# Kernel optimization log

Measured on AMD Instinct MI355X. Metric: run time of the kernel, lower is better.

## Reference

```python
import jax, jax.numpy as jnp
import numpy as np

B, T, C = 8, 2048, 512
H = 8
DH = C // H
MLP = 4 * C
EPS = 1e-5


def _ln(x, w, b):
    m = jnp.mean(x, axis=-1, keepdims=True)
    v = jnp.mean(jnp.square(x - m), axis=-1, keepdims=True)
    return (x - m) * jax.lax.rsqrt(v + EPS) * w + b


def setup_inputs() -> dict:
    key = jax.random.key(0)
    ks = jax.random.split(key, 12)
    s = 0.02
    return {
        "x": jax.random.normal(ks[0], (B, T, C), jnp.float32),
        "c": jax.random.normal(ks[1], (B, C), jnp.float32),
        "qkv_w": jax.random.normal(ks[2], (3 * C, C), jnp.float32) * s,
        "qkv_b": jnp.zeros((3 * C,), jnp.float32),
        "proj_w": jax.random.normal(ks[3], (C, C), jnp.float32) * s,
        "proj_b": jnp.zeros((C,), jnp.float32),
        "ada_w": jax.random.normal(ks[4], (6 * C, C), jnp.float32) * s,
        "ada_b": jnp.zeros((6 * C,), jnp.float32),
        "fc1_w": jax.random.normal(ks[5], (MLP, C), jnp.float32) * s,
        "fc1_b": jnp.zeros((MLP,), jnp.float32),
        "fc2_w": jax.random.normal(ks[6], (C, MLP), jnp.float32) * s,
        "fc2_b": jnp.zeros((C,), jnp.float32),
        "ln1_w": jnp.ones((C,), jnp.float32),
        "ln1_b": jnp.zeros((C,), jnp.float32),
        "ln2_w": jnp.ones((C,), jnp.float32),
        "ln2_b": jnp.zeros((C,), jnp.float32),
    }


def reference(x, c, qkv_w, qkv_b, proj_w, proj_b, ada_w, ada_b,
              fc1_w, fc1_b, fc2_w, fc2_b, ln1_w, ln1_b, ln2_w, ln2_b):
    # AdaLN modulation: SiLU -> Linear -> chunk into 6 [B,C] pieces
    mod = jax.nn.silu(c) @ ada_w.T + ada_b  # [B, 6C]
    sh_msa, sc_msa, g_msa, sh_mlp, sc_mlp, g_mlp = jnp.split(mod, 6, axis=1)

    # --- attention branch ---
    h = _ln(x, ln1_w, ln1_b) * (1.0 + sc_msa[:, None, :]) + sh_msa[:, None, :]
    qkv = h @ qkv_w.T + qkv_b  # [B, T, 3C]
    q, k, v = jnp.split(qkv, 3, axis=-1)
    q = q.reshape(B, T, H, DH).transpose(0, 2, 1, 3)  # [B,H,T,Dh]
    k = k.reshape(B, T, H, DH).transpose(0, 2, 1, 3)
    v = v.reshape(B, T, H, DH).transpose(0, 2, 1, 3)
    scores = jnp.einsum('bhqd,bhkd->bhqk', q, k) * (1.0 / np.sqrt(DH))
    w = jax.nn.softmax(scores, axis=-1)
    o = jnp.einsum('bhqk,bhkd->bhqd', w, v)  # [B,H,T,Dh]
    o = o.transpose(0, 2, 1, 3).reshape(B, T, C)
    attn = o @ proj_w.T + proj_b
    x = x + g_msa[:, None, :] * attn

    # --- MLP branch ---
    h2 = _ln(x, ln2_w, ln2_b) * (1.0 + sc_mlp[:, None, :]) + sh_mlp[:, None, :]
    m = jax.nn.gelu(h2 @ fc1_w.T + fc1_b, approximate=True) @ fc2_w.T + fc2_b
    return x + g_mlp[:, None, :] * m
```

## Files before the change

### kernel.cpp

```cpp
#include <hip/hip_runtime.h>
#include <cstdint>
#include <cstddef>

typedef unsigned short u16;
typedef short v8s __attribute__((ext_vector_type(8)));
typedef float v4f __attribute__((ext_vector_type(4)));
typedef float f32x16 __attribute__((ext_vector_type(16)));
typedef unsigned int v4u __attribute__((ext_vector_type(4)));
typedef unsigned short v4u16 __attribute__((ext_vector_type(4)));

#define TT 2048
#define CC 512

#define QSCALE 0.18033688011112042f

__device__ __forceinline__ u16 f2bf(float f) {
    unsigned u = __float_as_uint(f);
    u += 0x7fffu + ((u >> 16) & 1u);
    return (u16)(u >> 16);
}

__device__ __forceinline__ unsigned cvt_pk_bf16(float lo, float hi) {
    unsigned r;
    asm("v_cvt_pk_bf16_f32 %0, %1, %2" : "=v"(r) : "v"(lo), "v"(hi));
    return r;
}

__device__ __forceinline__ float fexp2(float x) {
    float xf = __builtin_floorf(x);
    float f = x - xf;
    float p = __builtin_fmaf(f, __builtin_fmaf(f, 0.343779f, 0.656213f), 1.0f);
    int e = (int)xf;
    return __uint_as_float(__float_as_uint(p) + ((unsigned)(e << 23)));
}

__device__ __forceinline__ void swap32(unsigned a, unsigned b, unsigned& x, unsigned& y) {
#if __has_builtin(__builtin_amdgcn_permlane32_swap)
    auto r = __builtin_amdgcn_permlane32_swap(a, b, false, false);
    x = r[0]; y = r[1];
#else
    unsigned bx = (unsigned)__shfl_xor((int)b, 32, 64);
    unsigned ax = (unsigned)__shfl_xor((int)a, 32, 64);
    bool hi5 = (threadIdx.x & 32) != 0;
    x = hi5 ? bx : a;
    y = hi5 ? b : ax;
#endif
}

__device__ __forceinline__ void gl2lds16(const void* g, void* l) {
    __builtin_amdgcn_global_load_lds(
        (const __attribute__((address_space(1))) unsigned int*)g,
        (__attribute__((address_space(3))) unsigned int*)l,
        16, 0, 0);
}

__global__ __launch_bounds__(256) void f2bf_all(const float* __restrict__ s0,
                                                const float* __restrict__ s1,
                                                const float* __restrict__ s2,
                                                const float* __restrict__ s3,
                                                u16* __restrict__ d) {
    int i = (blockIdx.x * 256 + threadIdx.x) * 4;
    const float* s; int off;
    if (i < 786432)       { s = s0; off = 0; }
    else if (i < 1048576) { s = s1; off = 786432; }
    else if (i < 2097152) { s = s2; off = 1048576; }
    else                  { s = s3; off = 2097152; }
    float4 v = *(const float4*)(s + (i - off));
    v4u16 r;
    r[0] = f2bf(v.x); r[1] = f2bf(v.y); r[2] = f2bf(v.z); r[3] = f2bf(v.w);
    *(v4u16*)(d + i) = r;
}

__global__ __launch_bounds__(256) void ada_kernel(const float* __restrict__ c,
                                                  const float* __restrict__ W,
                                                  const float* __restrict__ bias,
                                                  float* __restrict__ mod) {
    int idx = blockIdx.x * 4 + (threadIdx.x >> 6);
    int l = threadIdx.x & 63;
    int bb = idx / 3072;
    int n = idx - bb * 3072;
    const float* cp = c + bb * CC;
    const float* wp = W + (size_t)n * CC;
    float s = 0.f;
    #pragma unroll
    for (int i = 0; i < 8; ++i) {
        int k = l * 8 + i;
        float cv = cp[k];
        float sil = cv / (1.f + __expf(-cv));
        s += sil * wp[k];
    }
    #pragma unroll
    for (int off = 32; off; off >>= 1) s += __shfl_xor(s, off, 64);
    if (l == 0) mod[idx] = s + bias[n];
}

__global__ __launch_bounds__(256) void ln_mod_kernel(const float* __restrict__ X,
                                                     const float* __restrict__ lnw,
                                                     const float* __restrict__ lnb,
                                                     const float* __restrict__ mod,
                                                     int sh_off, int sc_off,
                                                     u16* __restrict__ out) {
    int row = blockIdx.x * 4 + (threadIdx.x >> 6);
    int l = threadIdx.x & 63;
    int b = row >> 11;
    const float* xr = X + (size_t)row * CC + l * 8;
    float4 va = *(const float4*)(xr);
    float4 vb = *(const float4*)(xr + 4);
    float v[8] = {va.x, va.y, va.z, va.w, vb.x, vb.y, vb.z, vb.w};
    float s = 0.f;
    #pragma unroll
    for (int i = 0; i < 8; ++i) s += v[i];
    #pragma unroll
    for (int off = 32; off; off >>= 1) s += __shfl_xor(s, off, 64);
    float mean = s * (1.f / CC);
    float q = 0.f;
    #pragma unroll
    for (int i = 0; i < 8; ++i) { float d = v[i] - mean; q += d * d; }
    #pragma unroll
    for (int off = 32; off; off >>= 1) q += __shfl_xor(q, off, 64);
    float rstd = rsqrtf(q * (1.f / CC) + 1e-5f);
    int col = l * 8;
    const float* shp = mod + b * 3072 + sh_off + col;
    const float* scp = mod + b * 3072 + sc_off + col;
    v8s st;
    #pragma unroll
    for (int i = 0; i < 8; ++i) {
        float hv = (v[i] - mean) * rstd * lnw[col + i] + lnb[col + i];
        float r = hv * (1.f + scp[i]) + shp[i];
        st[i] = (short)f2bf(r);
    }
    *(v8s*)(out + (size_t)row * CC + col) = st;
}

__global__ __launch_bounds__(512) void vt_kernel(const u16* __restrict__ qkv,
                                                 u16* __restrict__ vT) {
    __shared__ u16 tile[64 * 72];
    const int id = blockIdx.x;
    const int bh = id >> 5, tt = id & 31;
    const int b = bh >> 3, h = bh & 7;
    const int tid = threadIdx.x;
    const int tr = tid >> 3, d0 = (tid & 7) * 8;
    v8s v = *(const v8s*)(qkv + (size_t)(b * TT + tt * 64 + tr) * 1536 + 1024 + h * 64 + d0);
    *(v8s*)(&tile[tr * 72 + d0]) = v;
    __syncthreads();
    const int dr = tid >> 3, t0 = (tid & 7) * 8;
    v8s ov;
    #pragma unroll
    for (int e = 0; e < 8; ++e) ov[e] = (short)tile[(t0 + e) * 72 + dr];
    *(v8s*)(vT + (size_t)(bh * 64 + dr) * TT + tt * 64 + t0) = ov;
}

template <int MODE>
__global__ __launch_bounds__(512, 4)
void gemm_bt(const u16* __restrict__ A, const u16* __restrict__ W,
             const float* __restrict__ bias, void* __restrict__ outp,
             const float* __restrict__ resid, const float* __restrict__ gate,
             int NX, int N, int K) {
    __shared__ alignas(16) u16 Al[2][8192];
    __shared__ alignas(16) u16 Bl[2][4096];
    const int id = blockIdx.x;
    const int wg = (id & 7) * (gridDim.x >> 3) + (id >> 3);
    const int by = wg / NX, bx = wg - by * NX;
    const int bn = bx << 7, bm = by << 8;
    const int tid = threadIdx.x;
    const int w = tid >> 6, l = tid & 63;
    const int hi = l >> 4, lo = l & 15;
    const int wr = (w >> 1) << 6, wc = (w & 1) << 6;

    v4f acc[4][4] = {};

    const int srow = l >> 2;
    const int sp = l & 3;
    const int NT = K >> 5;

    auto stage = [&](int buf, int kt) {
        const int k0 = kt << 5;
        #pragma unroll
        for (int i = 0; i < 2; ++i) {
            const int c = w + (i << 3);
            const int row = (c << 4) + srow;
            const int lg = sp ^ ((row >> 1) & 3);
            gl2lds16(A + (size_t)(bm + row) * K + k0 + (lg << 3), &Al[buf][c << 9]);
        }
        {
            const int row = (w << 4) + srow;
            const int lg = sp ^ ((row >> 1) & 3);
            gl2lds16(W + (size_t)(bn + row) * K + k0 + (lg << 3), &Bl[buf][w << 9]);
        }
    };

    stage(0, 0);
    __syncthreads();
    int cur = 0;
    for (int t = 0; t < NT; ++t) {
        if (t + 1 < NT) stage(cur ^ 1, t + 1);
        const u16* Ab = Al[cur];
        const u16* Bb = Bl[cur];
        v8s aF[4], bF[4];
        #pragma unroll
        for (int mi = 0; mi < 4; ++mi) {
            int r = wr + (mi << 4) + lo;
            aF[mi] = *(const v8s*)(Ab + (r << 5) + ((hi ^ ((r >> 1) & 3)) << 3));
        }
        #pragma unroll
        for (int ni = 0; ni < 4; ++ni) {
            int r = wc + (ni << 4) + lo;
            bF[ni] = *(const v8s*)(Bb + (r << 5) + ((hi ^ ((r >> 1) & 3)) << 3));
        }
        #pragma unroll
        for (int mi = 0; mi < 4; ++mi)
            #pragma unroll
            for (int ni = 0; ni < 4; ++ni)
                acc[mi][ni] = __builtin_amdgcn_mfma_f32_16x16x32_bf16(
                    aF[mi], bF[ni], acc[mi][ni], 0, 0, 0);
        __syncthreads();
        cur ^= 1;
    }

    #pragma unroll
    for (int mi = 0; mi < 4; ++mi) {
        #pragma unroll
        for (int ni = 0; ni < 4; ++ni) {
            int col = bn + wc + (ni << 4) + lo;
            float bv = bias[col];
            #pragma unroll
            for (int j = 0; j < 4; ++j) {
                int row = bm + wr + (mi << 4) + hi * 4 + j;
                float v = acc[mi][ni][j] + bv;
                if constexpr (MODE == 0) {
                    float sc2 = (col < 512) ? QSCALE : 1.0f;
                    ((u16*)outp)[(size_t)row * N + col] = f2bf(v * sc2);
                } else if constexpr (MODE == 1) {
                    float u2 = 1.5957691216057308f * (v + 0.044715f * v * v * v);
                    float g = v / (1.f + __expf(-u2));
                    ((u16*)outp)[(size_t)row * N + col] = f2bf(g);
                } else {
                    float r = resid[(size_t)row * N + col];
                    float gt = gate[(row >> 11) * 3072 + col];
                    ((float*)outp)[(size_t)row * N + col] = r + gt * v;
                }
            }
        }
    }
}

__global__ __launch_bounds__(512, 4)
void attn_kernel(const u16* __restrict__ qkv, const u16* __restrict__ vT,
                 u16* __restrict__ O) {
    __shared__ alignas(16) u16 smem[18432];
    const int tid = threadIdx.x;
    const int w = tid >> 6, l = tid & 63;
    const int l31 = l & 31, l5 = l >> 5;
    const int id = blockIdx.x;
    const int bh = id & 63, b = bh >> 3, h = bh & 7;
    const int qt = id >> 6;

    const int qrow = qt * 256 + w * 32 + l31;
    const u16* qp = qkv + (size_t)(b * TT + qrow) * 1536 + h * 64;
    v8s qf[4];
    #pragma unroll
    for (int ks = 0; ks < 4; ++ks) qf[ks] = *(const v8s*)(qp + ks * 16 + l5 * 8);

    const int r8 = l >> 3;
    const int kc = (l & 7) ^ r8 ^ w;
    const u16* kptr = qkv + (size_t)(b * TT + 8 * w + r8) * 1536 + 512 + h * 64 + kc * 8;
    const u16* vptr = vT + (size_t)(bh * 64 + 8 * w + r8) * TT + kc * 8;

    auto stageKV = [&](int it, int buf) {
        gl2lds16(kptr + (size_t)it * 64 * 1536, smem + buf * 4096 + w * 512);
        gl2lds16(vptr + it * 64, smem + 8192 + buf * 4096 + w * 512);
    };

    const char* sbase = (const char*)smem;
    int offs[8];
    #pragma unroll
    for (int t = 0; t < 2; ++t)
        #pragma unroll
        for (int ks = 0; ks < 4; ++ks) {
            int row = t * 32 + l31;
            int phys = ((ks << 1) + l5) ^ (row & 7) ^ ((row >> 3) & 7);
            offs[t * 4 + ks] = row * 128 + phys * 16;
        }

    v8s onesf;
    #pragma unroll
    for (int i = 0; i < 8; ++i) onesf[i] = (short)0x3F80;

    stageKV(0, 0);
    __syncthreads();

    f32x16 o[2] = {};
    f32x16 lacc = {};

    #pragma unroll 2
    for (int it = 0; it < 32; ++it) {
        const int cur = it & 1;
        if (it + 1 < 32) stageKV(it + 1, cur ^ 1);
        const int koff = cur * 8192;

        f32x16 st[2];
        st[0] = (f32x16)0.f; st[1] = (f32x16)0.f;
        __builtin_amdgcn_s_setprio(1);
        #pragma unroll
        for (int ks = 0; ks < 4; ++ks) {
            v8s k0 = *(const v8s*)(sbase + offs[ks] + koff);
            v8s k1 = *(const v8s*)(sbase + offs[4 + ks] + koff);
            st[0] = __builtin_amdgcn_mfma_f32_32x32x16_bf16(k0, qf[ks], st[0], 0, 0, 0);
            st[1] = __builtin_amdgcn_mfma_f32_32x32x16_bf16(k1, qf[ks], st[1], 0, 0, 0);
        }
        __builtin_amdgcn_s_setprio(0);

        #pragma unroll
        for (int t2 = 0; t2 < 2; ++t2)
            #pragma unroll
            for (int r = 0; r < 16; ++r)
                st[t2][r] = fexp2(st[t2][r]);

        __builtin_amdgcn_s_setprio(1);
        #pragma unroll
        for (int ks = 0; ks < 4; ++ks) {
            const int tt = ks >> 1, rb = (ks & 1) * 8;
            unsigned pkA = cvt_pk_bf16(st[tt][rb + 0], st[tt][rb + 1]);
            unsigned pkB = cvt_pk_bf16(st[tt][rb + 4], st[tt][rb + 5]);
            unsigned pkC = cvt_pk_bf16(st[tt][rb + 2], st[tt][rb + 3]);
            unsigned pkD = cvt_pk_bf16(st[tt][rb + 6], st[tt][rb + 7]);
            unsigned w0, w1, w2, w3;
            swap32(pkA, pkB, w0, w2);
            swap32(pkC, pkD, w1, w3);
            v4u pw; pw[0] = w0; pw[1] = w1; pw[2] = w2; pw[3] = w3;
            v8s pa = __builtin_bit_cast(v8s, pw);
            v8s vf0 = *(const v8s*)(sbase + offs[ks] + koff + 16384);
            v8s vf1 = *(const v8s*)(sbase + offs[4 + ks] + koff + 16384);
            o[0] = __builtin_amdgcn_mfma_f32_32x32x16_bf16(vf0, pa, o[0], 0, 0, 0);
            o[1] = __builtin_amdgcn_mfma_f32_32x32x16_bf16(vf1, pa, o[1], 0, 0, 0);
            lacc = __builtin_amdgcn_mfma_f32_32x32x16_bf16(onesf, pa, lacc, 0, 0, 0);
        }
        __builtin_amdgcn_s_setprio(0);
        __syncthreads();
    }

    float inv = 1.f / lacc[0];
    char* outw = (char*)smem + w * 4608;
    #pragma unroll
    for (int t2 = 0; t2 < 2; ++t2)
        #pragma unroll
        for (int r = 0; r < 16; r += 2) {
            int dh = t2 * 32 + (r & 3) + ((r >> 2) << 3) + (l5 << 2);
            unsigned pk = cvt_pk_bf16(o[t2][r] * inv, o[t2][r + 1] * inv);
            *(unsigned*)(outw + l31 * 144 + dh * 2) = pk;
        }
    __syncthreads();
    #pragma unroll
    for (int i = 0; i < 4; ++i) {
        int idx = (i << 9) + tid;
        int qq = idx >> 3, cch = idx & 7;
        v8s vd = *(const v8s*)((char*)smem + (qq >> 5) * 4608 + (qq & 31) * 144 + cch * 16);
        *(v8s*)(O + (size_t)(b * TT + qt * 256 + qq) * 512 + h * 64 + cch * 8) = vd;
    }
}

extern "C" void kernel_launch(void* const* d_in, const int* in_sizes, int n_in,
                              void* d_out, int out_size, void* d_ws, size_t ws_size,
                              hipStream_t stream) {
    const float* x = (const float*)d_in[0];
    const float* c = (const float*)d_in[1];
    const float* qkv_w = (const float*)d_in[2];
    const float* qkv_b = (const float*)d_in[3];
    const float* proj_w = (const float*)d_in[4];
    const float* proj_b = (const float*)d_in[5];
    const float* ada_w = (const float*)d_in[6];
    const float* ada_b = (const float*)d_in[7];
    const float* fc1_w = (const float*)d_in[8];
    const float* fc1_b = (const float*)d_in[9];
    const float* fc2_w = (const float*)d_in[10];
    const float* fc2_b = (const float*)d_in[11];
    const float* ln1_w = (const float*)d_in[12];
    const float* ln1_b = (const float*)d_in[13];
    const float* ln2_w = (const float*)d_in[14];
    const float* ln2_b = (const float*)d_in[15];

    char* p = (char*)d_ws;
    auto carve = [&](size_t bytes) -> char* {
        char* r = p;
        p += (bytes + 255) & ~(size_t)255;
        return r;
    };
    float* mod  = (float*)carve((size_t)8 * 3072 * 4);
    u16* hbuf   = (u16*)carve((size_t)16384 * 512 * 2);
    u16* qkvb   = (u16*)carve((size_t)16384 * 1536 * 2);
    u16* attno  = (u16*)carve((size_t)16384 * 512 * 2);
    float* x1   = (float*)carve((size_t)16384 * 512 * 4);
    u16* wall   = (u16*)carve((size_t)3145728 * 2);
    u16* wq  = wall;
    u16* wpj = wall + 786432;
    u16* w1  = wall + 1048576;
    u16* w2  = wall + 2097152;
    u16* fc1g = qkvb;
    u16* vT   = hbuf;

    f2bf_all<<<3072, 256, 0, stream>>>(qkv_w, proj_w, fc1_w, fc2_w, wall);

    ada_kernel<<<24576 / 4, 256, 0, stream>>>(c, ada_w, ada_b, mod);

    ln_mod_kernel<<<16384 / 4, 256, 0, stream>>>(x, ln1_w, ln1_b, mod, 0, 512, hbuf);
    gemm_bt<0><<<64 * 12, 512, 0, stream>>>(hbuf, wq, qkv_b, qkvb,
                                            nullptr, nullptr, 12, 1536, 512);
    vt_kernel<<<64 * 32, 512, 0, stream>>>(qkvb, vT);
    attn_kernel<<<512, 512, 0, stream>>>(qkvb, vT, attno);
    gemm_bt<2><<<64 * 4, 512, 0, stream>>>(attno, wpj, proj_b, x1,
                                           x, mod + 2 * 512, 4, 512, 512);

    ln_mod_kernel<<<16384 / 4, 256, 0, stream>>>(x1, ln2_w, ln2_b, mod, 3 * 512, 4 * 512, hbuf);
    gemm_bt<1><<<64 * 16, 512, 0, stream>>>(hbuf, w1, fc1_b, fc1g,
                                            nullptr, nullptr, 16, 2048, 512);
    gemm_bt<2><<<64 * 4, 512, 0, stream>>>(fc1g, w2, fc2_b, (float*)d_out,
                                           x1, mod + 5 * 512, 4, 512, 2048);
}
```

Baseline: 309.6 us.

## Fuse V transpose into QKV GEMM epilogue and add smaller-tile GEMM

```diff
diff --git a/kernel.cpp b/kernel.cpp
--- a/kernel.cpp
+++ b/kernel.cpp
@@ -132,30 +132,11 @@
     *(v8s*)(out + (size_t)row * CC + col) = st;
 }
 
-__global__ __launch_bounds__(512) void vt_kernel(const u16* __restrict__ qkv,
-                                                 u16* __restrict__ vT) {
-    __shared__ u16 tile[64 * 72];
-    const int id = blockIdx.x;
-    const int bh = id >> 5, tt = id & 31;
-    const int b = bh >> 3, h = bh & 7;
-    const int tid = threadIdx.x;
-    const int tr = tid >> 3, d0 = (tid & 7) * 8;
-    v8s v = *(const v8s*)(qkv + (size_t)(b * TT + tt * 64 + tr) * 1536 + 1024 + h * 64 + d0);
-    *(v8s*)(&tile[tr * 72 + d0]) = v;
-    __syncthreads();
-    const int dr = tid >> 3, t0 = (tid & 7) * 8;
-    v8s ov;
-    #pragma unroll
-    for (int e = 0; e < 8; ++e) ov[e] = (short)tile[(t0 + e) * 72 + dr];
-    *(v8s*)(vT + (size_t)(bh * 64 + dr) * TT + tt * 64 + t0) = ov;
-}
-
 template <int MODE>
 __global__ __launch_bounds__(512, 4)
-void gemm_bt(const u16* __restrict__ A, const u16* __restrict__ W,
-             const float* __restrict__ bias, void* __restrict__ outp,
-             const float* __restrict__ resid, const float* __restrict__ gate,
-             int NX, int N, int K) {
+void gemm_big(const u16* __restrict__ A, const u16* __restrict__ W,
+              const float* __restrict__ bias, u16* __restrict__ outp,
+              u16* __restrict__ vTp, int NX, int N, int K) {
     __shared__ alignas(16) u16 Al[2][8192];
     __shared__ alignas(16) u16 Bl[2][4096];
     const int id = blockIdx.x;
@@ -223,22 +204,113 @@
         for (int ni = 0; ni < 4; ++ni) {
             int col = bn + wc + (ni << 4) + lo;
             float bv = bias[col];
+            if constexpr (MODE == 0) {
+                if (col >= 1024) {
+                    int d = col - 1024;
+                    int row0 = bm + wr + (mi << 4) + hi * 4;
+                    v4u16 pk;
+                    #pragma unroll
+                    for (int j = 0; j < 4; ++j) pk[j] = f2bf(acc[mi][ni][j] + bv);
+                    size_t addr = ((size_t)((row0 >> 11) * 8 + (d >> 6)) * 64 + (d & 63)) * TT
+                                  + (row0 & 2047);
+                    *(v4u16*)(vTp + addr) = pk;
+                } else {
+                    float sc2 = (col < 512) ? QSCALE : 1.0f;
+                    #pragma unroll
+                    for (int j = 0; j < 4; ++j) {
+                        int row = bm + wr + (mi << 4) + hi * 4 + j;
+                        outp[(size_t)row * N + col] = f2bf((acc[mi][ni][j] + bv) * sc2);
+                    }
+                }
+            } else {
+                #pragma unroll
+                for (int j = 0; j < 4; ++j) {
+                    int row = bm + wr + (mi << 4) + hi * 4 + j;
+                    float v = acc[mi][ni][j] + bv;
+                    float u2 = 1.5957691216057308f * (v + 0.044715f * v * v * v);
+                    float g = v / (1.f + __expf(-u2));
+                    outp[(size_t)row * N + col] = f2bf(g);
+                }
+            }
+        }
+    }
+}
+
+__global__ __launch_bounds__(256)
+void gemm_sm(const u16* __restrict__ A, const u16* __restrict__ W,
+             const float* __restrict__ bias, float* __restrict__ outp,
+             const float* __restrict__ resid, const float* __restrict__ gate,
+             int NX, int N, int K) {
+    __shared__ alignas(16) u16 Al[2][4096];
+    __shared__ alignas(16) u16 Bl[2][4096];
+    const int id = blockIdx.x;
+    const int wg = (id & 7) * (gridDim.x >> 3) + (id >> 3);
+    const int by = wg / NX, bx = wg - by * NX;
+    const int bn = bx << 7, bm = by << 7;
+    const int tid = threadIdx.x;
+    const int w = tid >> 6, l = tid & 63;
+    const int hi = l >> 4, lo = l & 15;
+    const int wr = (w >> 1) << 6, wc = (w & 1) << 6;
+
+    v4f acc[4][4] = {};
+
+    const int srow = l >> 2;
+    const int sp = l & 3;
+    const int NT = K >> 5;
+
+    auto stage = [&](int buf, int kt) {
+        const int k0 = kt << 5;
+        #pragma unroll
+        for (int i = 0; i < 2; ++i) {
+            const int c = w + (i << 2);
+            const int row = (c << 4) + srow;
+            const int lg = sp ^ ((row >> 1) & 3);
+            gl2lds16(A + (size_t)(bm + row) * K + k0 + (lg << 3), &Al[buf][c << 9]);
+            gl2lds16(W + (size_t)(bn + row) * K + k0 + (lg << 3), &Bl[buf][c << 9]);
+        }
+    };
+
+    stage(0, 0);
+    __syncthreads();
+    int cur = 0;
+    for (int t = 0; t < NT; ++t) {
+        if (t + 1 < NT) stage(cur ^ 1, t + 1);
+        const u16* Ab = Al[cur];
+        const u16* Bb = Bl[cur];
+        v8s aF[4], bF[4];
+        #pragma unroll
+        for (int mi = 0; mi < 4; ++mi) {
+            int r = wr + (mi << 4) + lo;
+            aF[mi] = *(const v8s*)(Ab + (r << 5) + ((hi ^ ((r >> 1) & 3)) << 3));
+        }
+        #pragma unroll
+        for (int ni = 0; ni < 4; ++ni) {
+            int r = wc + (ni << 4) + lo;
+            bF[ni] = *(const v8s*)(Bb + (r << 5) + ((hi ^ ((r >> 1) & 3)) << 3));
+        }
+        #pragma unroll
+        for (int mi = 0; mi < 4; ++mi)
+            #pragma unroll
+            for (int ni = 0; ni < 4; ++ni)
+                acc[mi][ni] = __builtin_amdgcn_mfma_f32_16x16x32_bf16(
+                    aF[mi], bF[ni], acc[mi][ni], 0, 0, 0);
+        __syncthreads();
+        cur ^= 1;
+    }
+
+    #pragma unroll
+    for (int mi = 0; mi < 4; ++mi) {
+        #pragma unroll
+        for (int ni = 0; ni < 4; ++ni) {
+            int col = bn + wc + (ni << 4) + lo;
+            float bv = bias[col];
             #pragma unroll
             for (int j = 0; j < 4; ++j) {
                 int row = bm + wr + (mi << 4) + hi * 4 + j;
                 float v = acc[mi][ni][j] + bv;
-                if constexpr (MODE == 0) {
-                    float sc2 = (col < 512) ? QSCALE : 1.0f;
-                    ((u16*)outp)[(size_t)row * N + col] = f2bf(v * sc2);
-                } else if constexpr (MODE == 1) {
-                    float u2 = 1.5957691216057308f * (v + 0.044715f * v * v * v);
-                    float g = v / (1.f + __expf(-u2));
-                    ((u16*)outp)[(size_t)row * N + col] = f2bf(g);
-                } else {
-                    float r = resid[(size_t)row * N + col];
-                    float gt = gate[(row >> 11) * 3072 + col];
-                    ((float*)outp)[(size_t)row * N + col] = r + gt * v;
-                }
+                float r = resid[(size_t)row * N + col];
+                float gt = gate[(row >> 11) * 3072 + col];
+                outp[(size_t)row * N + col] = r + gt * v;
             }
         }
     }
@@ -311,10 +383,11 @@
         __builtin_amdgcn_s_setprio(0);
 
         #pragma unroll
-        for (int t2 = 0; t2 < 2; ++t2)
-            #pragma unroll
-            for (int r = 0; r < 16; ++r)
-                st[t2][r] = fexp2(st[t2][r]);
+        for (int r = 0; r < 16; ++r)
+            st[0][r] = __builtin_exp2f(st[0][r]);
+        #pragma unroll
+        for (int r = 0; r < 16; ++r)
+            st[1][r] = fexp2(st[1][r]);
 
         __builtin_amdgcn_s_setprio(1);
         #pragma unroll
@@ -396,23 +469,22 @@
     u16* w1  = wall + 1048576;
     u16* w2  = wall + 2097152;
     u16* fc1g = qkvb;
-    u16* vT   = hbuf;
+    u16* vT   = (u16*)x1;
 
     f2bf_all<<<3072, 256, 0, stream>>>(qkv_w, proj_w, fc1_w, fc2_w, wall);
 
     ada_kernel<<<24576 / 4, 256, 0, stream>>>(c, ada_w, ada_b, mod);
 
     ln_mod_kernel<<<16384 / 4, 256, 0, stream>>>(x, ln1_w, ln1_b, mod, 0, 512, hbuf);
-    gemm_bt<0><<<64 * 12, 512, 0, stream>>>(hbuf, wq, qkv_b, qkvb,
-                                            nullptr, nullptr, 12, 1536, 512);
-    vt_kernel<<<64 * 32, 512, 0, stream>>>(qkvb, vT);
+    gemm_big<0><<<64 * 12, 512, 0, stream>>>(hbuf, wq, qkv_b, qkvb, vT,
+                                             12, 1536, 512);
     attn_kernel<<<512, 512, 0, stream>>>(qkvb, vT, attno);
-    gemm_bt<2><<<64 * 4, 512, 0, stream>>>(attno, wpj, proj_b, x1,
-                                           x, mod + 2 * 512, 4, 512, 512);
+    gemm_sm<<<4 * 128, 256, 0, stream>>>(attno, wpj, proj_b, x1,
+                                         x, mod + 2 * 512, 4, 512, 512);
 
     ln_mod_kernel<<<16384 / 4, 256, 0, stream>>>(x1, ln2_w, ln2_b, mod, 3 * 512, 4 * 512, hbuf);
-    gemm_bt<1><<<64 * 16, 512, 0, stream>>>(hbuf, w1, fc1_b, fc1g,
-                                            nullptr, nullptr, 16, 2048, 512);
-    gemm_bt<2><<<64 * 4, 512, 0, stream>>>(fc1g, w2, fc2_b, (float*)d_out,
-                                           x1, mod + 5 * 512, 4, 512, 2048);
-}
+    gemm_big<1><<<64 * 16, 512, 0, stream>>>(hbuf, w1, fc1_b, fc1g, nullptr,
+                                             16, 2048, 512);
+    gemm_sm<<<4 * 128, 256, 0, stream>>>(fc1g, w2, fc2_b, (float*)d_out,
+                                         x1, mod + 5 * 512, 4, 512, 2048);
+}
```

After: 295.3 us. -4.6%, faster.
